# Kernel optimization log

Hardware: AMD Instinct MI355X
Metric: run time of the kernel (lower is better)

The kernel has to match this reference:

```python
import jax, jax.numpy as jnp
import numpy as np

N, D1, D2, B = 8, 2048, 1024, 512
D = D1 * D2
MAXBW = 3
NUM_PART = 5          # num_possible_partitions
TEMP = 0.01           # TEMPERATURE used in df_lt
DENOS = (3.0, 5.0, 17.0)  # 2^2-1, 2^2+1, 2^4+1


def ste_floor(x):
    # straight-through floor: forward floor, backward identity
    return x + jax.lax.stop_gradient(jnp.floor(x) - x)


def segmented_mean(piece, scheme, msp):
    """Replicates the inner python scan over sorted rows.
    piece:  (N, D) sorted residual errors
    scheme: (N-1, D) rounded split decisions (0/1), per column
    msp:    (N-1, D) soft split probabilities (grad factors), per column
    Returns (N, D): each row gets grad_ * (segment mean) of its segment.
    """
    n = piece.shape[0]
    buf = jnp.zeros_like(piece[0])
    cnt = jnp.zeros_like(piece[0])
    g = jnp.ones_like(piece[0])
    reset = jnp.zeros(piece.shape[1], dtype=bool)
    vlist, blist = [], []
    for i in range(n):
        buf = jnp.where(reset, piece[i], buf + piece[i])
        cnt = jnp.where(reset, 1.0, cnt + 1.0)
        g = jnp.where(reset, 1.0, g)
        if i == n - 1:
            vlist.append(g * (buf / cnt))
            blist.append(jnp.ones_like(reset))
        else:
            b = scheme[i] > 0.5
            vlist.append(jnp.where(b, g * msp[i], 0.0) * (buf / cnt))
            blist.append(b)
            g = jnp.where(b, g, g * (1.0 - msp[i]))
            reset = b
    # broadcast each segment-end value back to all rows of its segment
    out = vlist[-1]
    outs = [out]
    for i in range(n - 2, -1, -1):
        out = jnp.where(blist[i], vlist[i], out)
        outs.append(out)
    return jnp.stack(outs[::-1], axis=0)


def residual_quant(U, vsum, s, thr):
    """One residual quantization level (the update_partition=True branch)."""
    res = U - vsum                                   # (N, D)
    idx_maps = jnp.argsort(res, axis=0)              # torch.sort ascending, dim=0
    sorted_err = jnp.take_along_axis(res, idx_maps, axis=0)
    delta = sorted_err[1:] - sorted_err[:-1]         # (N-1, D), >= 0
    delta = delta / jnp.max(delta)
    msp = jax.nn.sigmoid((delta - thr) / TEMP)       # mean_split_point (N-1, D)
    rs = jnp.round(msp)                              # round_split, 0/1

    nm1 = N - 1
    P = 2 ** nm1  # all possible split-column patterns (torch.unique over dim=1)
    weights = (2 ** jnp.arange(nm1 - 1, -1, -1)).astype(jnp.int32)  # row 0 = MSB (lexicographic)
    code = jnp.sum(rs.astype(jnp.int32) * weights[:, None], axis=0)  # (D,)
    counts = jnp.zeros((P,), jnp.int32).at[code].add(1)
    present = counts > 0
    # torch.unique sorts patterns lexicographically -> rank = #present codes below
    rank_of_code = jnp.cumsum(present.astype(jnp.int32)) - present.astype(jnp.int32)
    order = jnp.argsort(-counts)                     # codes by count descending
    top_codes = order[:NUM_PART]
    top_ranks = rank_of_code[top_codes]              # s_indices[:NUM_PART]
    # binary patterns for every possible code
    patterns = ((jnp.arange(P)[:, None] >> jnp.arange(nm1 - 1, -1, -1)[None, :]) & 1).astype(jnp.float32)  # (P, N-1)
    inter = patterns @ patterns[top_codes].T         # (P, NUM_PART)
    sel = jnp.argmax(inter, axis=1)
    reassigned = top_ranks[sel]                      # (P,)
    is_top = jnp.any(rank_of_code[:, None] == top_ranks[None, :], axis=1)
    final_rank = jnp.where(is_top, rank_of_code, reassigned)  # (P,)
    c_rank = final_rank[code]                        # clustered_indices, (D,)

    # NOTE: original indexes round_split / mean_split_point columns BY the
    # unique-cluster index value s_idx (a quirk of the source); replicate it.
    scheme_used = rs[:, c_rank]                      # (N-1, D)
    msp_used = msp[:, c_rank]                        # (N-1, D)

    inner = segmented_mean(sorted_err, scheme_used, msp_used)  # (N, D)
    # einsum('cb,cba->ab', inner, one_hot(idx_maps)) == unsort along dim 0
    inv = jnp.argsort(idx_maps, axis=0)
    grouped = jnp.take_along_axis(inner, inv, axis=0)
    return s * ste_floor(grouped / s)


def setup_inputs():
    key = jax.random.key(0)
    k1, k2 = jax.random.split(key)
    x = jax.random.normal(k1, (B, N, D1), dtype=jnp.float32)
    # kaiming_normal_ on (N, D): std = sqrt(2 / fan_in), fan_in = D
    U = jax.random.normal(k2, (N, D), dtype=jnp.float32) * np.float32(np.sqrt(2.0 / D))
    thres_mean = jnp.full((D2,), -1.3, dtype=jnp.float32)
    return {"x": x, "U": U, "thres_mean": thres_mean}


def reference(x, U, thres_mean):
    beta = jnp.max(U)
    alpha = jnp.min(U)
    s = (beta - alpha) / DENOS[0]
    vsum = s * ste_floor(U / s)                      # base quantization level
    thr = jax.nn.sigmoid(jnp.repeat(thres_mean, D1))  # thres_mean.repeat_interleave(D1)
    for deno in DENOS[1:MAXBW]:
        s = s / deno
        vsum = vsum + residual_quant(U, vsum, s, thr)
    w = vsum.reshape(N, D1, D2)
    return jnp.einsum('bnd,ndl->bnl', x, w)
```

## Files before the change

### kernel.cpp

```cpp
#include <hip/hip_runtime.h>
#include <hip/hip_bf16.h>
#include <math.h>

#define NROW 8
#define DT   2097152
#define DD1  2048
#define DD2  1024
#define BATCH 512
#define NBLK4 2048
#define NBLK2 4096


typedef __attribute__((ext_vector_type(8))) short short8;
typedef __attribute__((ext_vector_type(4))) float f32x4;

__device__ __forceinline__ unsigned fenc(float f){
  unsigned u = __float_as_uint(f);
  return (u & 0x80000000u) ? ~u : (u | 0x80000000u);
}
__device__ __forceinline__ float fdec(unsigned k){
  return (k & 0x80000000u) ? __uint_as_float(k ^ 0x80000000u) : __uint_as_float(~k);
}
__device__ __forceinline__ float sigmoid_ref(float z){
  #pragma clang fp contract(off)
  return 1.0f / (1.0f + expf(-z));
}
__device__ __forceinline__ unsigned short f2bf(float f){
  __hip_bfloat16 h = __float2bfloat16(f);
  return *reinterpret_cast<unsigned short*>(&h);
}
__device__ __forceinline__ void async16(const unsigned short* g, unsigned short* l){
  __builtin_amdgcn_global_load_lds((const __attribute__((address_space(1))) unsigned int*)g,
                                   (__attribute__((address_space(3))) unsigned int*)l, 16, 0, 0);
}

#define CSWAPV(a,b) { float _lo=fminf(a,b), _hi=fmaxf(a,b); a=_lo; b=_hi; }
__device__ __forceinline__ void sort8v(float v[8]){
  CSWAPV(v[0],v[1]) CSWAPV(v[2],v[3]) CSWAPV(v[4],v[5]) CSWAPV(v[6],v[7])
  CSWAPV(v[0],v[2]) CSWAPV(v[1],v[3]) CSWAPV(v[4],v[6]) CSWAPV(v[5],v[7])
  CSWAPV(v[1],v[2]) CSWAPV(v[5],v[6])
  CSWAPV(v[0],v[4]) CSWAPV(v[1],v[5]) CSWAPV(v[2],v[6]) CSWAPV(v[3],v[7])
  CSWAPV(v[2],v[4]) CSWAPV(v[3],v[5])
  CSWAPV(v[1],v[2]) CSWAPV(v[3],v[4]) CSWAPV(v[5],v[6])
}
__device__ __forceinline__ void cswapkv(float&av,int&ai,float&bv,int&bi){
  bool sw = (av > bv) || ((av == bv) && (ai > bi));
  float nav = sw ? bv : av; float nbv = sw ? av : bv;
  int   nai = sw ? bi : ai; int   nbi = sw ? ai : bi;
  av = nav; bv = nbv; ai = nai; bi = nbi;
}
#define CSWAPK(i,j) cswapkv(v[i],ix[i],v[j],ix[j]);
__device__ __forceinline__ void sort8kv(float v[8], int ix[8]){
  CSWAPK(0,1) CSWAPK(2,3) CSWAPK(4,5) CSWAPK(6,7)
  CSWAPK(0,2) CSWAPK(1,3) CSWAPK(4,6) CSWAPK(5,7)
  CSWAPK(1,2) CSWAPK(5,6)
  CSWAPK(0,4) CSWAPK(1,5) CSWAPK(2,6) CSWAPK(3,7)
  CSWAPK(2,4) CSWAPK(3,5)
  CSWAPK(1,2) CSWAPK(3,4) CSWAPK(5,6)
}

__global__ void k_init(unsigned* __restrict__ meta){
  int t = threadIdx.x;
  if (t == 0){ meta[0] = 0u; meta[1] = 0xFFFFFFFFu; meta[2] = 0u; meta[3] = 0u; }
  if (t < 128){ meta[4+t] = 0u; meta[132+t] = 0u; }
}

__global__ __launch_bounds__(256) void k_minmax(const float* __restrict__ U, unsigned* __restrict__ meta){
  __shared__ unsigned smx[256], smn[256];
  int t = threadIdx.x;
  size_t i = (size_t)blockIdx.x*256 + t;
  size_t stride = (size_t)gridDim.x*256;
  const float4* U4 = (const float4*)U;
  float mx = -INFINITY, mn = INFINITY;
  for (; i < (size_t)NROW*DT/4; i += stride){
    float4 v = U4[i];
    mx = fmaxf(fmaxf(mx,v.x), fmaxf(v.y, fmaxf(v.z,v.w)));
    mn = fminf(fminf(mn,v.x), fminf(v.y, fminf(v.z,v.w)));
  }
  smx[t] = fenc(mx); smn[t] = fenc(mn);
  __syncthreads();
  for (int o = 128; o > 0; o >>= 1){
    if (t < o){ smx[t] = max(smx[t], smx[t+o]); smn[t] = min(smn[t], smn[t+o]); }
    __syncthreads();
  }
  if (t == 0){ atomicMax(&meta[0], smx[0]); atomicMin(&meta[1], smn[0]); }
}

__global__ __launch_bounds__(256) void k_passA2(const float* __restrict__ U, unsigned* __restrict__ meta){
  #pragma clang fp contract(off)
  __shared__ unsigned sred[256];
  int t = threadIdx.x;
  int d0 = (blockIdx.x*256 + t)*4;
  float beta = fdec(meta[0]), alpha = fdec(meta[1]);
  float s1 = (beta - alpha) / 3.0f;
  float4 u[8];
  #pragma unroll
  for (int i = 0; i < 8; ++i) u[i] = *(const float4*)(U + (size_t)i*DT + d0);
  unsigned dmax = 0u;
  #pragma unroll
  for (int c = 0; c < 4; ++c){
    float res[8];
    #pragma unroll
    for (int i = 0; i < 8; ++i){
      float uv = ((const float*)&u[i])[c];
      res[i] = uv - s1*floorf(uv/s1);
    }
    sort8v(res);
    float m = 0.0f;
    #pragma unroll
    for (int i = 0; i < 7; ++i) m = fmaxf(m, res[i+1] - res[i]);
    dmax = max(dmax, __float_as_uint(m));
  }
  sred[t] = dmax;
  __syncthreads();
  for (int o = 128; o > 0; o >>= 1){
    if (t < o) sred[t] = max(sred[t], sred[t+o]);
    __syncthreads();
  }
  if (t == 0) atomicMax(&meta[2], sred[0]);
}

template<int LEVEL>
__global__ __launch_bounds__(256) void k_passB(const float* __restrict__ U, const float* __restrict__ vsum,
                                               const float* __restrict__ thres_mean,
                                               unsigned char* __restrict__ code, unsigned* __restrict__ meta){
  #pragma clang fp contract(off)
  __shared__ int hist[128];
  int t = threadIdx.x;
  if (t < 128) hist[t] = 0;
  __syncthreads();
  int d0 = (blockIdx.x*256 + t)*4;
  float beta = fdec(meta[0]), alpha = fdec(meta[1]);
  float s1 = (beta - alpha) / 3.0f;
  float gmax = __uint_as_float(meta[(LEVEL==2)?2:3]);
  float4 u[8], b[8];
  #pragma unroll
  for (int i = 0; i < 8; ++i){
    u[i] = *(const float4*)(U + (size_t)i*DT + d0);
    if (LEVEL == 2){
      float4 bb;
      bb.x = s1*floorf(u[i].x/s1); bb.y = s1*floorf(u[i].y/s1);
      bb.z = s1*floorf(u[i].z/s1); bb.w = s1*floorf(u[i].w/s1);
      b[i] = bb;
    } else {
      b[i] = *(const float4*)(vsum + (size_t)i*DT + d0);
    }
  }
  float thr = sigmoid_ref(thres_mean[d0 >> 11]);
  uchar4 cods;
  unsigned char* cp = (unsigned char*)&cods;
  #pragma unroll
  for (int c = 0; c < 4; ++c){
    float res[8];
    #pragma unroll
    for (int i = 0; i < 8; ++i) res[i] = ((const float*)&u[i])[c] - ((const float*)&b[i])[c];
    sort8v(res);
    int cd = 0;
    #pragma unroll
    for (int i = 0; i < 7; ++i){
      float dn  = (res[i+1] - res[i]) / gmax;
      float z   = (dn - thr) / 0.01f;
      float msp = sigmoid_ref(z);
      int bit = (int)rintf(msp);
      cd = (cd << 1) | bit;
    }
    cp[c] = (unsigned char)cd;
    atomicAdd(&hist[cd], 1);
  }
  *(uchar4*)(code + d0) = cods;
  __syncthreads();
  if (t < 128 && hist[t] > 0) atomicAdd((int*)&meta[((LEVEL==2)?4:132) + t], hist[t]);
}

template<int LEVEL>
__global__ void k_small(const float* __restrict__ U, const float* __restrict__ vsum,
                        const float* __restrict__ thres_mean, unsigned* __restrict__ meta){
  #pragma clang fp contract(off)
  __shared__ int cs[128], rk[128], redk[128];
  __shared__ int top_code[5], top_rank[5];
  __shared__ int w0cnt;
  int c = threadIdx.x;
  cs[c] = (int)meta[((LEVEL==2)?4:132) + c];
  bool present = cs[c] > 0;
  unsigned long long bm = __ballot(present);
  int lane = c & 63;
  int r = (int)__popcll(bm & ((1ull << lane) - 1ull));
  if (c == 63) w0cnt = (int)__popcll(bm);
  __syncthreads();
  if (c >= 64) r += w0cnt;
  rk[c] = r;
  __syncthreads();
  for (int k = 0; k < 5; ++k){
    redk[c] = (cs[c] << 7) | (127 - c);
    __syncthreads();
    for (int o = 64; o > 0; o >>= 1){
      if (c < o) redk[c] = max(redk[c], redk[c+o]);
      __syncthreads();
    }
    if (c == 0){
      int best = 127 - (redk[0] & 127);
      top_code[k] = best; top_rank[k] = rk[best];
      cs[best] = -1;
    }
    __syncthreads();
  }
  int besti = -1, sel = 0;
  #pragma unroll
  for (int j = 0; j < 5; ++j){
    int inter = __popc(c & top_code[j]);
    if (inter > besti){ besti = inter; sel = j; }
  }
  bool is_top = false;
  #pragma unroll
  for (int j = 0; j < 5; ++j) is_top = is_top || (rk[c] == top_rank[j]);
  int fr = is_top ? rk[c] : top_rank[sel];
  ((int*)meta)[260 + c] = fr;
  float beta = fdec(meta[0]), alpha = fdec(meta[1]);
  float s1 = (beta - alpha) / 3.0f;
  float gmax = __uint_as_float(meta[(LEVEL==2)?2:3]);
  float res[8];
  #pragma unroll
  for (int i = 0; i < 8; ++i){
    size_t off = (size_t)i*DT + c;
    float u = U[off];
    float b = (LEVEL==2) ? s1*floorf(u/s1) : vsum[off];
    res[i] = u - b;
  }
  sort8v(res);
  float thr = sigmoid_ref(thres_mean[c >> 11]);
  unsigned bits = 0;
  float* msp_tab = (float*)&meta[388];
  #pragma unroll
  for (int i = 0; i < 7; ++i){
    float dn  = (res[i+1] - res[i]) / gmax;
    float z   = (dn - thr) / 0.01f;
    float msp = sigmoid_ref(z);
    msp_tab[c*7 + i] = msp;
    bits |= ((unsigned)(int)rintf(msp)) << i;
  }
  meta[1284 + c] = bits;
}

template<int LEVEL>
__global__ __launch_bounds__(256) void k_passD(const float* __restrict__ U, float* __restrict__ vsum,
                                               const unsigned char* __restrict__ code,
                                               unsigned* __restrict__ meta){
  #pragma clang fp contract(off)
  __shared__ int fr_s[128];
  __shared__ unsigned bits_s[128];
  __shared__ float msp_s[128*7];
  __shared__ unsigned sred[256];
  int t = threadIdx.x;
  if (t < 128){ fr_s[t] = ((int*)meta)[260 + t]; bits_s[t] = meta[1284 + t]; }
  for (int i = t; i < 128*7; i += 256) msp_s[i] = ((float*)&meta[388])[i];
  __syncthreads();
  int d0 = (blockIdx.x*256 + t)*2;
  float beta = fdec(meta[0]), alpha = fdec(meta[1]);
  float s1 = (beta - alpha) / 3.0f;
  float s2 = s1 / 5.0f;
  float s  = (LEVEL == 2) ? s2 : (s2 / 17.0f);
  float2 u2[8], b2[8];
  #pragma unroll
  for (int i = 0; i < 8; ++i){
    u2[i] = *(const float2*)(U + (size_t)i*DT + d0);
    if (LEVEL == 2){
      b2[i].x = s1*floorf(u2[i].x/s1);
      b2[i].y = s1*floorf(u2[i].y/s1);
    } else {
      b2[i] = *(const float2*)(vsum + (size_t)i*DT + d0);
    }
  }
  unsigned char cd2[2];
  *(ushort*)cd2 = *(const ushort*)(code + d0);
  float vnew[2][8];
  unsigned dmax = 0u;
  #pragma unroll
  for (int c = 0; c < 2; ++c){
    float v[8]; int ix[8];
    #pragma unroll
    for (int i = 0; i < 8; ++i){
      v[i] = ((const float*)&u2[i])[c] - ((const float*)&b2[i])[c];
      ix[i] = i;
    }
    sort8kv(v, ix);
    int cr = fr_s[cd2[c]];
    unsigned sb = bits_s[cr];
    float vv[8]; bool bl[8];
    float buf = 0.0f, cnt = 0.0f, g = 1.0f; bool reset = false;
    #pragma unroll
    for (int i = 0; i < 8; ++i){
      buf = reset ? v[i] : (buf + v[i]);
      cnt = reset ? 1.0f : (cnt + 1.0f);
      g   = reset ? 1.0f : g;
      float m = buf / cnt;
      if (i == 7){ vv[7] = g * m; bl[7] = true; }
      else {
        float msp = msp_s[cr*7 + i];
        bool b = ((sb >> i) & 1u) != 0u;
        vv[i] = b ? ((g * msp) * m) : 0.0f;
        bl[i] = b;
        g = b ? g : (g * (1.0f - msp));
        reset = b;
      }
    }
    float out = vv[7];
    float inner[8];
    inner[7] = out;
    for (int i = 6; i >= 0; --i){ if (bl[i]) out = vv[i]; inner[i] = out; }
    float res3[8];
    #pragma unroll
    for (int rr = 0; rr < 8; ++rr){
      float innr = inner[0];
      #pragma unroll
      for (int i = 0; i < 8; ++i) innr = (ix[i] == rr) ? inner[i] : innr;
      float vn = ((const float*)&b2[rr])[c] + s * floorf(innr / s);
      vnew[c][rr] = vn;
      if (LEVEL == 2) res3[rr] = ((const float*)&u2[rr])[c] - vn;
    }
    if (LEVEL == 2){
      sort8v(res3);
      float m = 0.0f;
      #pragma unroll
      for (int i = 0; i < 7; ++i) m = fmaxf(m, res3[i+1] - res3[i]);
      dmax = max(dmax, __float_as_uint(m));
    }
  }
  #pragma unroll
  for (int rr = 0; rr < 8; ++rr){
    float2 o; o.x = vnew[0][rr]; o.y = vnew[1][rr];
    *(float2*)(vsum + (size_t)rr*DT + d0) = o;
  }
  if (LEVEL == 2){
    sred[t] = dmax;
    __syncthreads();
    for (int o = 128; o > 0; o >>= 1){
      if (t < o) sred[t] = max(sred[t], sred[t+o]);
      __syncthreads();
    }
    if (t == 0) atomicMax(&meta[3], sred[0]);
  }
}

__global__ __launch_bounds__(256) void k_wt(const float* __restrict__ vsum, unsigned short* __restrict__ wt){
  __shared__ unsigned short tile[64][68];
  int t = threadIdx.x;
  int c4 = t & 15, r0 = t >> 4;
  int n = blockIdx.z, k0 = blockIdx.y*64, l0 = blockIdx.x*64;
  const float* src = vsum + (size_t)n*DT;
  #pragma unroll
  for (int i = 0; i < 4; ++i){
    int r = r0 + i*16;
    float4 v = *(const float4*)(src + (size_t)(k0+r)*DD2 + l0 + c4*4);
    tile[r][c4*4+0] = f2bf(v.x); tile[r][c4*4+1] = f2bf(v.y);
    tile[r][c4*4+2] = f2bf(v.z); tile[r][c4*4+3] = f2bf(v.w);
  }
  __syncthreads();
  unsigned short* dst = wt + (size_t)n*DT;
  #pragma unroll
  for (int i = 0; i < 4; ++i){
    int rl = r0 + i*16;
    ushort4 o;
    o.x = tile[c4*4+0][rl]; o.y = tile[c4*4+1][rl];
    o.z = tile[c4*4+2][rl]; o.w = tile[c4*4+3][rl];
    *(ushort4*)(dst + (size_t)(l0+rl)*DD1 + k0 + c4*4) = o;
  }
}

__global__ __launch_bounds__(256) void k_xb(const float* __restrict__ x, unsigned short* __restrict__ xb){
  int idx = (blockIdx.x*256 + threadIdx.x)*4;
  float4 v = *(const float4*)(x + idx);
  ushort4 o;
  o.x = f2bf(v.x); o.y = f2bf(v.y); o.z = f2bf(v.z); o.w = f2bf(v.w);
  *(ushort4*)(xb + idx) = o;
}

__global__ __launch_bounds__(256) void k_gemm(const unsigned short* __restrict__ xb,
                                              const unsigned short* __restrict__ wt,
                                              float* __restrict__ out){
  __shared__ __align__(16) unsigned short As[64*64];
  __shared__ __align__(16) unsigned short Bs[128*64];
  int t = threadIdx.x;
  int lane = t & 63, wv = t >> 6;
  int n  = blockIdx.z;
  int b0 = blockIdx.y * 64;
  int l0 = blockIdx.x * 128;
  int wm = (wv >> 1) * 32, wn = (wv & 1) * 64;
  int col = lane & 15, quad = lane >> 4;
  int arow = lane >> 3, aseg = lane & 7;
  const unsigned short* wtn = wt + (size_t)n*DT;
  f32x4 acc[2][4] = {};
  for (int k0 = 0; k0 < DD1; k0 += 64){
    #pragma unroll
    for (int i = 0; i < 2; ++i){
      int row = wv*16 + i*8 + arow;
      const unsigned short* g = xb + (((size_t)(b0+row)*NROW + n)*DD1 + k0 + aseg*8);
      async16(g, &As[(wv*16 + i*8)*64]);
    }
    #pragma unroll
    for (int i = 0; i < 4; ++i){
      int row = wv*32 + i*8 + arow;
      const unsigned short* g = wtn + ((size_t)(l0+row)*DD1 + k0 + aseg*8);
      async16(g, &Bs[(wv*32 + i*8)*64]);
    }
    __syncthreads();
    #pragma unroll
    for (int ks = 0; ks < 2; ++ks){
      int kq = ks*32 + quad*8;
      short8 af[2], bfr[4];
      #pragma unroll
      for (int mi = 0; mi < 2; ++mi) af[mi]  = *(const short8*)&As[(wm + mi*16 + col)*64 + kq];
      #pragma unroll
      for (int ni = 0; ni < 4; ++ni) bfr[ni] = *(const short8*)&Bs[(wn + ni*16 + col)*64 + kq];
      #pragma unroll
      for (int mi = 0; mi < 2; ++mi)
        #pragma unroll
        for (int ni = 0; ni < 4; ++ni)
          acc[mi][ni] = __builtin_amdgcn_mfma_f32_16x16x32_bf16(af[mi], bfr[ni], acc[mi][ni], 0, 0, 0);
    }
    __syncthreads();
  }
  #pragma unroll
  for (int mi = 0; mi < 2; ++mi)
    #pragma unroll
    for (int ni = 0; ni < 4; ++ni)
      #pragma unroll
      for (int r = 0; r < 4; ++r){
        int b = b0 + wm + mi*16 + quad*4 + r;
        int l = l0 + wn + ni*16 + col;
        out[((size_t)b*NROW + n)*DD2 + l] = acc[mi][ni][r];
      }
}

extern "C" void kernel_launch(void* const* d_in, const int* in_sizes, int n_in,
                              void* d_out, int out_size, void* d_ws, size_t ws_size,
                              hipStream_t stream){
  const float* x  = (const float*)d_in[0];
  const float* U  = (const float*)d_in[1];
  const float* tm = (const float*)d_in[2];
  float* out  = (float*)d_out;
  float* vsum = (float*)d_ws;
  unsigned char* code = (unsigned char*)d_ws + (size_t)NROW*DT*4;
  unsigned short* wt  = (unsigned short*)((unsigned char*)d_ws + (size_t)NROW*DT*4 + DT);
  unsigned* meta = (unsigned*)((unsigned char*)d_ws + (size_t)NROW*DT*4 + DT + (size_t)NROW*DT*2);
  unsigned short* xb = (unsigned short*)d_ws;
  (void)in_sizes; (void)n_in; (void)out_size; (void)ws_size;

  k_init  <<<1,    256, 0, stream>>>(meta);
  k_minmax<<<2048, 256, 0, stream>>>(U, meta);

  k_passA2  <<<NBLK4, 256, 0, stream>>>(U, meta);
  k_passB<2><<<NBLK4, 256, 0, stream>>>(U, vsum, tm, code, meta);
  k_small<2><<<1,    128, 0, stream>>>(U, vsum, tm, meta);
  k_passD<2><<<NBLK2, 256, 0, stream>>>(U, vsum, code, meta);

  k_passB<3><<<NBLK4, 256, 0, stream>>>(U, vsum, tm, code, meta);
  k_small<3><<<1,    128, 0, stream>>>(U, vsum, tm, meta);
  k_passD<3><<<NBLK2, 256, 0, stream>>>(U, vsum, code, meta);

  k_wt  <<<dim3(DD2/64, DD1/64, NROW), 256, 0, stream>>>(vsum, wt);
  k_xb  <<<(BATCH*NROW*DD1)/1024, 256, 0, stream>>>(x, xb);
  k_gemm<<<dim3(DD2/128, BATCH/64, NROW), 256, 0, stream>>>(xb, wt, out);
}
```

Measured before the change: 475.9 us.

## Use reciprocal multiplies, threshold compare, and LDS unsort in quantization passes

Replaces divisions by s1, gmax and s with multiplies by precomputed reciprocals. The sigmoid-and-round split test becomes a direct compare of the normalized gap against the threshold. passD now handles four columns per thread with float4 loads and stores, and does the unsort scatter through a 32 KB LDS buffer instead of a select chain. The reciprocal math and the compare shortcut can change floor and rounding results at boundaries compared with the reference, and the larger LDS footprint may reduce occupancy.

```diff
diff --git a/kernel.cpp b/kernel.cpp
--- a/kernel.cpp
+++ b/kernel.cpp
@@ -8,7 +8,6 @@
 #define DD2  1024
 #define BATCH 512
 #define NBLK4 2048
-#define NBLK2 4096
 
 
 typedef __attribute__((ext_vector_type(8))) short short8;
@@ -28,6 +27,10 @@
 __device__ __forceinline__ unsigned short f2bf(float f){
   __hip_bfloat16 h = __float2bfloat16(f);
   return *reinterpret_cast<unsigned short*>(&h);
+}
+__device__ __forceinline__ float base1(float u, float s1, float inv_s1){
+  #pragma clang fp contract(off)
+  return s1 * floorf(u * inv_s1);
 }
 __device__ __forceinline__ void async16(const unsigned short* g, unsigned short* l){
   __builtin_amdgcn_global_load_lds((const __attribute__((address_space(1))) unsigned int*)g,
@@ -93,6 +96,7 @@
   int d0 = (blockIdx.x*256 + t)*4;
   float beta = fdec(meta[0]), alpha = fdec(meta[1]);
   float s1 = (beta - alpha) / 3.0f;
+  float inv_s1 = 1.0f / s1;
   float4 u[8];
   #pragma unroll
   for (int i = 0; i < 8; ++i) u[i] = *(const float4*)(U + (size_t)i*DT + d0);
@@ -103,7 +107,7 @@
     #pragma unroll
     for (int i = 0; i < 8; ++i){
       float uv = ((const float*)&u[i])[c];
-      res[i] = uv - s1*floorf(uv/s1);
+      res[i] = uv - base1(uv, s1, inv_s1);
     }
     sort8v(res);
     float m = 0.0f;
@@ -132,15 +136,17 @@
   int d0 = (blockIdx.x*256 + t)*4;
   float beta = fdec(meta[0]), alpha = fdec(meta[1]);
   float s1 = (beta - alpha) / 3.0f;
+  float inv_s1 = 1.0f / s1;
   float gmax = __uint_as_float(meta[(LEVEL==2)?2:3]);
+  float inv_gmax = 1.0f / gmax;
   float4 u[8], b[8];
   #pragma unroll
   for (int i = 0; i < 8; ++i){
     u[i] = *(const float4*)(U + (size_t)i*DT + d0);
     if (LEVEL == 2){
       float4 bb;
-      bb.x = s1*floorf(u[i].x/s1); bb.y = s1*floorf(u[i].y/s1);
-      bb.z = s1*floorf(u[i].z/s1); bb.w = s1*floorf(u[i].w/s1);
+      bb.x = base1(u[i].x, s1, inv_s1); bb.y = base1(u[i].y, s1, inv_s1);
+      bb.z = base1(u[i].z, s1, inv_s1); bb.w = base1(u[i].w, s1, inv_s1);
       b[i] = bb;
     } else {
       b[i] = *(const float4*)(vsum + (size_t)i*DT + d0);
@@ -158,10 +164,8 @@
     int cd = 0;
     #pragma unroll
     for (int i = 0; i < 7; ++i){
-      float dn  = (res[i+1] - res[i]) / gmax;
-      float z   = (dn - thr) / 0.01f;
-      float msp = sigmoid_ref(z);
-      int bit = (int)rintf(msp);
+      float dn = (res[i+1] - res[i]) * inv_gmax;
+      int bit = (dn > thr) ? 1 : 0;
       cd = (cd << 1) | bit;
     }
     cp[c] = (unsigned char)cd;
@@ -217,13 +221,14 @@
   ((int*)meta)[260 + c] = fr;
   float beta = fdec(meta[0]), alpha = fdec(meta[1]);
   float s1 = (beta - alpha) / 3.0f;
+  float inv_s1 = 1.0f / s1;
   float gmax = __uint_as_float(meta[(LEVEL==2)?2:3]);
   float res[8];
   #pragma unroll
   for (int i = 0; i < 8; ++i){
     size_t off = (size_t)i*DT + c;
     float u = U[off];
-    float b = (LEVEL==2) ? s1*floorf(u/s1) : vsum[off];
+    float b = (LEVEL==2) ? base1(u, s1, inv_s1) : vsum[off];
     res[i] = u - b;
   }
   sort8v(res);
@@ -246,6 +251,7 @@
                                                const unsigned char* __restrict__ code,
                                                unsigned* __restrict__ meta){
   #pragma clang fp contract(off)
+  __shared__ float q_lds[32*256];
   __shared__ int fr_s[128];
   __shared__ unsigned bits_s[128];
   __shared__ float msp_s[128*7];
@@ -254,36 +260,38 @@
   if (t < 128){ fr_s[t] = ((int*)meta)[260 + t]; bits_s[t] = meta[1284 + t]; }
   for (int i = t; i < 128*7; i += 256) msp_s[i] = ((float*)&meta[388])[i];
   __syncthreads();
-  int d0 = (blockIdx.x*256 + t)*2;
+  int d0 = (blockIdx.x*256 + t)*4;
   float beta = fdec(meta[0]), alpha = fdec(meta[1]);
   float s1 = (beta - alpha) / 3.0f;
+  float inv_s1 = 1.0f / s1;
   float s2 = s1 / 5.0f;
   float s  = (LEVEL == 2) ? s2 : (s2 / 17.0f);
-  float2 u2[8], b2[8];
+  float inv_s = 1.0f / s;
+  float4 u4[8], b4[8];
   #pragma unroll
   for (int i = 0; i < 8; ++i){
-    u2[i] = *(const float2*)(U + (size_t)i*DT + d0);
+    u4[i] = *(const float4*)(U + (size_t)i*DT + d0);
     if (LEVEL == 2){
-      b2[i].x = s1*floorf(u2[i].x/s1);
-      b2[i].y = s1*floorf(u2[i].y/s1);
+      float4 bb;
+      bb.x = base1(u4[i].x, s1, inv_s1); bb.y = base1(u4[i].y, s1, inv_s1);
+      bb.z = base1(u4[i].z, s1, inv_s1); bb.w = base1(u4[i].w, s1, inv_s1);
+      b4[i] = bb;
     } else {
-      b2[i] = *(const float2*)(vsum + (size_t)i*DT + d0);
-    }
-  }
-  unsigned char cd2[2];
-  *(ushort*)cd2 = *(const ushort*)(code + d0);
-  float vnew[2][8];
-  unsigned dmax = 0u;
-  #pragma unroll
-  for (int c = 0; c < 2; ++c){
+      b4[i] = *(const float4*)(vsum + (size_t)i*DT + d0);
+    }
+  }
+  uchar4 cods = *(const uchar4*)(code + d0);
+  const unsigned char* cp = (const unsigned char*)&cods;
+  #pragma unroll
+  for (int c = 0; c < 4; ++c){
     float v[8]; int ix[8];
     #pragma unroll
     for (int i = 0; i < 8; ++i){
-      v[i] = ((const float*)&u2[i])[c] - ((const float*)&b2[i])[c];
+      v[i] = ((const float*)&u4[i])[c] - ((const float*)&b4[i])[c];
       ix[i] = i;
     }
     sort8kv(v, ix);
-    int cr = fr_s[cd2[c]];
+    int cr = fr_s[cp[c]];
     unsigned sb = bits_s[cr];
     float vv[8]; bool bl[8];
     float buf = 0.0f, cnt = 0.0f, g = 1.0f; bool reset = false;
@@ -292,7 +300,7 @@
       buf = reset ? v[i] : (buf + v[i]);
       cnt = reset ? 1.0f : (cnt + 1.0f);
       g   = reset ? 1.0f : g;
-      float m = buf / cnt;
+      float m = buf * __builtin_amdgcn_rcpf(cnt);
       if (i == 7){ vv[7] = g * m; bl[7] = true; }
       else {
         float msp = msp_s[cr*7 + i];
@@ -307,15 +315,23 @@
     float inner[8];
     inner[7] = out;
     for (int i = 6; i >= 0; --i){ if (bl[i]) out = vv[i]; inner[i] = out; }
+    #pragma unroll
+    for (int i = 0; i < 8; ++i){
+      float q = s * floorf(inner[i] * inv_s);
+      q_lds[(ix[i]*4 + c)*256 + t] = q;
+    }
+  }
+  float4 vn4[8];
+  unsigned dmax = 0u;
+  #pragma unroll
+  for (int c = 0; c < 4; ++c){
     float res3[8];
     #pragma unroll
     for (int rr = 0; rr < 8; ++rr){
-      float innr = inner[0];
-      #pragma unroll
-      for (int i = 0; i < 8; ++i) innr = (ix[i] == rr) ? inner[i] : innr;
-      float vn = ((const float*)&b2[rr])[c] + s * floorf(innr / s);
-      vnew[c][rr] = vn;
-      if (LEVEL == 2) res3[rr] = ((const float*)&u2[rr])[c] - vn;
+      float q = q_lds[(rr*4 + c)*256 + t];
+      float vn = ((const float*)&b4[rr])[c] + q;
+      ((float*)&vn4[rr])[c] = vn;
+      if (LEVEL == 2) res3[rr] = ((const float*)&u4[rr])[c] - vn;
     }
     if (LEVEL == 2){
       sort8v(res3);
@@ -326,10 +342,8 @@
     }
   }
   #pragma unroll
-  for (int rr = 0; rr < 8; ++rr){
-    float2 o; o.x = vnew[0][rr]; o.y = vnew[1][rr];
-    *(float2*)(vsum + (size_t)rr*DT + d0) = o;
-  }
+  for (int rr = 0; rr < 8; ++rr)
+    *(float4*)(vsum + (size_t)rr*DT + d0) = vn4[rr];
   if (LEVEL == 2){
     sred[t] = dmax;
     __syncthreads();
@@ -451,11 +465,11 @@
   k_passA2  <<<NBLK4, 256, 0, stream>>>(U, meta);
   k_passB<2><<<NBLK4, 256, 0, stream>>>(U, vsum, tm, code, meta);
   k_small<2><<<1,    128, 0, stream>>>(U, vsum, tm, meta);
-  k_passD<2><<<NBLK2, 256, 0, stream>>>(U, vsum, code, meta);
+  k_passD<2><<<NBLK4, 256, 0, stream>>>(U, vsum, code, meta);
 
   k_passB<3><<<NBLK4, 256, 0, stream>>>(U, vsum, tm, code, meta);
   k_small<3><<<1,    128, 0, stream>>>(U, vsum, tm, meta);
-  k_passD<3><<<NBLK2, 256, 0, stream>>>(U, vsum, code, meta);
+  k_passD<3><<<NBLK4, 256, 0, stream>>>(U, vsum, code, meta);
 
   k_wt  <<<dim3(DD2/64, DD1/64, NROW), 256, 0, stream>>>(vsum, wt);
   k_xb  <<<(BATCH*NROW*DD1)/1024, 256, 0, stream>>>(x, xb);
```

Result: faster. 428.7 us (-9.9%).
